# Kernel optimization log

Measured on AMD Instinct MI355X. Metric: run time of the kernel, lower is better.

## Reference

```python
import jax, jax.numpy as jnp
import numpy as np
from math import sqrt

B, S, D_MODEL = 2, 2048, 1024
H = 16
ADIM = D_MODEL // H  # 64
K_REL = 16
N_PEMB = 2 * K_REL + 1  # 33, bidirectional rel-pos vocabulary


def setup_inputs() -> dict:
    key = jax.random.key(0)
    ks = jax.random.split(key, 8)
    sc = 0.02
    return {
        "iQ": jax.random.normal(ks[0], (B, S, D_MODEL), jnp.float32),
        "iK": jax.random.normal(ks[1], (B, S, D_MODEL), jnp.float32),
        "iV": jax.random.normal(ks[2], (B, S, D_MODEL), jnp.float32),
        "Wq": jax.random.normal(ks[3], (D_MODEL, D_MODEL), jnp.float32) * sc,
        "Wk": jax.random.normal(ks[4], (D_MODEL, D_MODEL), jnp.float32) * sc,
        "Wv": jax.random.normal(ks[5], (D_MODEL, D_MODEL), jnp.float32) * sc,
        "Wo": jax.random.normal(ks[6], (D_MODEL, D_MODEL), jnp.float32) * sc,
        "rel_pemb": jax.random.normal(ks[7], (N_PEMB, ADIM), jnp.float32) * sc,
    }


def reference(iQ, iK, iV, Wq, Wk, Wv, Wo, rel_pemb):
    b, nq, _ = iQ.shape
    seql = iK.shape[1]
    # projections -> [b, h, len, d]
    q = (iQ @ Wq).reshape(b, nq, H, ADIM).transpose(0, 2, 1, 3)
    k = (iK @ Wk).reshape(b, seql, H, ADIM).transpose(0, 2, 1, 3)
    v = (iV @ Wv).reshape(b, seql, H, ADIM).transpose(0, 2, 1, 3)
    # content scores: [b, h, nq, seql]
    scores = jnp.einsum("bhqd,bhsd->bhqs", q, k)
    # relative position bias: rel[i, j] = clamp(j - i, -K, K) + K
    pos = jnp.arange(seql)
    rel = jnp.clip(pos[None, :] - pos[:, None], -K_REL, K_REL) + K_REL
    rel = rel[seql - nq:, :]  # narrow to query rows: [nq, seql]
    e = rel_pemb[rel]  # [nq, seql, d]
    scores = scores + jnp.einsum("bhqd,qsd->bhqs", q, e)
    scores = scores / sqrt(ADIM)
    attn = jax.nn.softmax(scores, axis=-1)
    ctx = jnp.einsum("bhqs,bhsd->bqhd", attn, v).reshape(b, nq, H * ADIM)
    return ctx @ Wo
```

## Files before the change

kernel.cpp:

```cpp
#include <hip/hip_runtime.h>
#include <hip/hip_bf16.h>

#define BB 2
#define S 2048
#define DM 1024
#define H 16
#define ADIM 64
#define NP 33

typedef __bf16 bf16x8 __attribute__((ext_vector_type(8)));
typedef float f32x4 __attribute__((ext_vector_type(4)));

__device__ __forceinline__ void gload16(const void* g, void* l) {
  __builtin_amdgcn_global_load_lds(
      (__attribute__((address_space(1))) void*)(g),
      (__attribute__((address_space(3))) void*)(l), 16, 0, 0);
}

__global__ __launch_bounds__(256) void wtrans(
    const float* __restrict__ W0, const float* __restrict__ W1,
    const float* __restrict__ W2, __bf16* __restrict__ T0,
    __bf16* __restrict__ T1, __bf16* __restrict__ T2) {
  const float* W; __bf16* T;
  switch (blockIdx.z) {
    case 0: W = W0; T = T0; break;
    case 1: W = W1; T = T1; break;
    default: W = W2; T = T2; break;
  }
  __shared__ __bf16 tile[64][65];
  int j = threadIdx.x & 63, i0 = threadIdx.x >> 6;
  int n0 = blockIdx.x * 64, k0 = blockIdx.y * 64;
#pragma unroll
  for (int p = 0; p < 16; ++p) {
    int i = i0 + p * 4;
    tile[i][j] = (__bf16)W[(size_t)(k0 + i) * DM + n0 + j];
  }
  __syncthreads();
#pragma unroll
  for (int p = 0; p < 16; ++p) {
    int i = i0 + p * 4;
    T[(size_t)(n0 + i) * DM + k0 + j] = tile[j][i];
  }
}

#define LDK 40
template <bool A_FP32, typename CT>
__device__ __forceinline__ void gemm_body(const void* __restrict__ Av,
                                          const __bf16* __restrict__ BT,
                                          CT* __restrict__ C, int mode) {
  __shared__ __align__(16) __bf16 As[128 * LDK];
  __shared__ __align__(16) __bf16 Bs[128 * 32];
  int t = threadIdx.x;
  int w = t >> 6, lane = t & 63, l15 = lane & 15, quad = lane >> 4;
  int wm = w >> 1, wn = w & 1;
  int i2 = blockIdx.x + (blockIdx.y << 3);
  int xcd = i2 & 7, slot = i2 >> 3;
  int m0 = (xcd + ((slot >> 3) << 3)) * 128;
  int n0 = (slot & 7) * 128;
  constexpr int LA = A_FP32 ? LDK : 32;
  f32x4 acc[4][4] = {};
  int lr = t >> 2;
  int lk = (t & 3) * 8;
  int r4 = lane >> 2;
  int c8 = (lane & 3) * 8;
  for (int k0 = 0; k0 < DM; k0 += 32) {
    if constexpr (A_FP32) {
#pragma unroll
      for (int rr = 0; rr < 2; ++rr) {
        int row = rr * 64 + lr;
        const float* src = (const float*)Av + (size_t)(m0 + row) * DM + k0 + lk;
        float4 a0 = *(const float4*)src;
        float4 a1 = *(const float4*)(src + 4);
        bf16x8 v;
        v[0] = (__bf16)a0.x; v[1] = (__bf16)a0.y;
        v[2] = (__bf16)a0.z; v[3] = (__bf16)a0.w;
        v[4] = (__bf16)a1.x; v[5] = (__bf16)a1.y;
        v[6] = (__bf16)a1.z; v[7] = (__bf16)a1.w;
        *(bf16x8*)&As[row * LDK + lk] = v;
      }
    } else {
#pragma unroll
      for (int q = 0; q < 2; ++q) {
        int half = w * 2 + q;
        gload16((const __bf16*)Av + (size_t)(m0 + half * 16 + r4) * DM + k0 + c8,
                &As[half * 512]);
      }
    }
#pragma unroll
    for (int q = 0; q < 2; ++q) {
      int half = w * 2 + q;
      gload16(&BT[(size_t)(n0 + half * 16 + r4) * DM + k0 + c8],
              &Bs[half * 512]);
    }
    __syncthreads();
    bf16x8 af[4], bfr[4];
#pragma unroll
    for (int mi = 0; mi < 4; ++mi)
      af[mi] = *(const bf16x8*)&As[(wm * 64 + mi * 16 + l15) * LA + quad * 8];
#pragma unroll
    for (int ni = 0; ni < 4; ++ni)
      bfr[ni] = *(const bf16x8*)&Bs[(wn * 64 + ni * 16 + l15) * 32 + quad * 8];
#pragma unroll
    for (int mi = 0; mi < 4; ++mi)
#pragma unroll
      for (int ni = 0; ni < 4; ++ni)
        acc[mi][ni] = __builtin_amdgcn_mfma_f32_16x16x32_bf16(
            af[mi], bfr[ni], acc[mi][ni], 0, 0, 0);
    __syncthreads();
  }
#pragma unroll
  for (int mi = 0; mi < 4; ++mi)
#pragma unroll
    for (int ni = 0; ni < 4; ++ni)
#pragma unroll
      for (int r = 0; r < 4; ++r) {
        int row = m0 + wm * 64 + mi * 16 + quad * 4 + r;
        int col = n0 + wn * 64 + ni * 16 + l15;
        CT v = (CT)acc[mi][ni][r];
        if (mode == 0) {
          C[(size_t)row * DM + col] = v;
        } else {
          int b = row >> 11, s = row & (S - 1);
          int h = col >> 6, d = col & (ADIM - 1);
          if (mode == 1)
            C[((size_t)(b * H + h) * S + s) * ADIM + d] = v;
          else
            C[((size_t)(b * H + h) * ADIM + d) * S + s] = v;
        }
      }
}

__global__ __launch_bounds__(256) void proj3(
    const float* __restrict__ iQ, const float* __restrict__ iK,
    const float* __restrict__ iV, const __bf16* __restrict__ WqT,
    const __bf16* __restrict__ WkT, const __bf16* __restrict__ WvT,
    __bf16* __restrict__ Qw, __bf16* __restrict__ Kw,
    __bf16* __restrict__ Vt) {
  const float* A; const __bf16* B; __bf16* C; int mode;
  switch (blockIdx.z) {
    case 0: A = iQ; B = WqT; C = Qw; mode = 1; break;
    case 1: A = iK; B = WkT; C = Kw; mode = 1; break;
    default: A = iV; B = WvT; C = Vt; mode = 2; break;
  }
  gemm_body<true, __bf16>(A, B, C, mode);
}

__global__ __launch_bounds__(256) void gemm_final(
    const __bf16* __restrict__ ctx, const __bf16* __restrict__ WoT,
    float* __restrict__ out) {
  gemm_body<false, float>(ctx, WoT, out, 0);
}

#define AST 72
__global__ __launch_bounds__(256) void attn_flash(
    const __bf16* __restrict__ Qw, const __bf16* __restrict__ Kw,
    const __bf16* __restrict__ Vt, const float* __restrict__ pemb,
    __bf16* __restrict__ ctx) {
  int bh = blockIdx.y, b = bh >> 4, h = bh & 15;
  int q0 = blockIdx.x * 64;
  int t = threadIdx.x, w = t >> 6, lane = t & 63, l15 = lane & 15,
      quad = lane >> 4;
  const __bf16* Qh = Qw + (size_t)bh * S * ADIM;
  const __bf16* Kh = Kw + (size_t)bh * S * ADIM;
  const __bf16* Vh = Vt + (size_t)bh * ADIM * S;

  __shared__ __align__(16) char smem[36352];
  __bf16* Ks = (__bf16*)smem;
  __bf16* Vs = (__bf16*)(smem + 9216);
  float* pband = (float*)(smem + 18432);
  __bf16* pbufw = (__bf16*)(smem + 27136 + w * 2304);
  __bf16* peb = (__bf16*)smem;

  for (int i = t; i < 48 * 64; i += 256) {
    int r = i >> 6, d = i & 63;
    peb[r * AST + d] = (r < NP) ? (__bf16)pemb[i] : (__bf16)0.f;
  }

  int qa = q0 + w * 16 + l15;
  bf16x8 qf0 = *(const bf16x8*)&Qh[(size_t)qa * ADIM + quad * 8];
  bf16x8 qf1 = *(const bf16x8*)&Qh[(size_t)qa * ADIM + 32 + quad * 8];
  __syncthreads();

  {
    f32x4 pc[3] = {};
#pragma unroll
    for (int ni = 0; ni < 3; ++ni) {
      bf16x8 b0 = *(const bf16x8*)&peb[(ni * 16 + l15) * AST + quad * 8];
      bf16x8 b1 = *(const bf16x8*)&peb[(ni * 16 + l15) * AST + 32 + quad * 8];
      pc[ni] = __builtin_amdgcn_mfma_f32_16x16x32_bf16(qf0, b0, pc[ni], 0, 0, 0);
      pc[ni] = __builtin_amdgcn_mfma_f32_16x16x32_bf16(qf1, b1, pc[ni], 0, 0, 0);
    }
#pragma unroll
    for (int ni = 0; ni < 3; ++ni)
#pragma unroll
      for (int r = 0; r < 4; ++r) {
        int col = ni * 16 + l15;
        if (col < NP) pband[(w * 16 + quad * 4 + r) * 34 + col] = pc[ni][r];
      }
  }
  __syncthreads();

  int qc = q0 + w * 16 + quad * 4;
  int lrow = w * 16 + quad * 4;
  int qw0 = q0 + w * 16;
  float lsum[4] = {0.f, 0.f, 0.f, 0.f};
  f32x4 o[4] = {};

  float blo[4], bhi[4];
#pragma unroll
  for (int r = 0; r < 4; ++r) {
    blo[r] = __expf(pband[(lrow + r) * 34 + 0] * 0.125f);
    bhi[r] = __expf(pband[(lrow + r) * 34 + 32] * 0.125f);
  }

  int srow = t >> 3;
  int scol = (t & 7) * 8;
  bf16x8 k0r = *(const bf16x8*)&Kh[(size_t)srow * ADIM + scol];
  bf16x8 k1r = *(const bf16x8*)&Kh[(size_t)(32 + srow) * ADIM + scol];
  bf16x8 v0r = *(const bf16x8*)&Vh[(size_t)srow * S + scol];
  bf16x8 v1r = *(const bf16x8*)&Vh[(size_t)(32 + srow) * S + scol];

  for (int s0 = 0; s0 < S; s0 += 64) {
    __syncthreads();
    *(bf16x8*)&Ks[srow * AST + scol] = k0r;
    *(bf16x8*)&Ks[(32 + srow) * AST + scol] = k1r;
    *(bf16x8*)&Vs[srow * AST + scol] = v0r;
    *(bf16x8*)&Vs[(32 + srow) * AST + scol] = v1r;
    int sn = s0 + 64;
    if (sn < S) {
      k0r = *(const bf16x8*)&Kh[(size_t)(sn + srow) * ADIM + scol];
      k1r = *(const bf16x8*)&Kh[(size_t)(sn + 32 + srow) * ADIM + scol];
      v0r = *(const bf16x8*)&Vh[(size_t)srow * S + sn + scol];
      v1r = *(const bf16x8*)&Vh[(size_t)(32 + srow) * S + sn + scol];
    }
    __syncthreads();

    f32x4 c[4];
#pragma unroll
    for (int j = 0; j < 4; ++j) {
      f32x4 cj = {};
      bf16x8 kb0 = *(const bf16x8*)&Ks[(j * 16 + l15) * AST + quad * 8];
      bf16x8 kb1 = *(const bf16x8*)&Ks[(j * 16 + l15) * AST + 32 + quad * 8];
      cj = __builtin_amdgcn_mfma_f32_16x16x32_bf16(qf0, kb0, cj, 0, 0, 0);
      cj = __builtin_amdgcn_mfma_f32_16x16x32_bf16(qf1, kb1, cj, 0, 0, 0);
      c[j] = cj;
    }

    float pv[4][4];
    bool below = (s0 + 79 <= qw0);
    bool above = (s0 >= qw0 + 31);
    if (below || above) {
#pragma unroll
      for (int j = 0; j < 4; ++j)
#pragma unroll
        for (int r = 0; r < 4; ++r) {
          float f = below ? blo[r] : bhi[r];
          float e = __expf(c[j][r] * 0.125f) * f;
          lsum[r] += e;
          pv[j][r] = e;
        }
    } else {
#pragma unroll
      for (int j = 0; j < 4; ++j)
#pragma unroll
        for (int r = 0; r < 4; ++r) {
          int qg = qc + r;
          int sg = s0 + j * 16 + l15;
          int i0 = sg - qg; i0 = i0 < -16 ? -16 : (i0 > 16 ? 16 : i0); i0 += 16;
          float e = __expf((c[j][r] + pband[(lrow + r) * 34 + i0]) * 0.125f);
          lsum[r] += e;
          pv[j][r] = e;
        }
    }

#pragma unroll
    for (int j = 0; j < 4; ++j)
#pragma unroll
      for (int r = 0; r < 4; ++r)
        pbufw[(quad * 4 + r) * AST + j * 16 + l15] = (__bf16)pv[j][r];
    bf16x8 pa0 = *(const bf16x8*)&pbufw[l15 * AST + quad * 8];
    bf16x8 pa1 = *(const bf16x8*)&pbufw[l15 * AST + 32 + quad * 8];

#pragma unroll
    for (int nt = 0; nt < 4; ++nt) {
      bf16x8 vb0 = *(const bf16x8*)&Vs[(nt * 16 + l15) * AST + quad * 8];
      bf16x8 vb1 = *(const bf16x8*)&Vs[(nt * 16 + l15) * AST + 32 + quad * 8];
      o[nt] = __builtin_amdgcn_mfma_f32_16x16x32_bf16(pa0, vb0, o[nt], 0, 0, 0);
      o[nt] = __builtin_amdgcn_mfma_f32_16x16x32_bf16(pa1, vb1, o[nt], 0, 0, 0);
    }
  }

#pragma unroll
  for (int r = 0; r < 4; ++r) {
#pragma unroll
    for (int mm = 1; mm < 16; mm <<= 1) lsum[r] += __shfl_xor(lsum[r], mm, 64);
  }
#pragma unroll
  for (int nt = 0; nt < 4; ++nt)
#pragma unroll
    for (int r = 0; r < 4; ++r) {
      int qg = qc + r;
      int d = nt * 16 + l15;
      ctx[(size_t)(b * S + qg) * DM + h * ADIM + d] =
          (__bf16)(o[nt][r] / lsum[r]);
    }
}

extern "C" void kernel_launch(void* const* d_in, const int* in_sizes, int n_in,
                              void* d_out, int out_size, void* d_ws,
                              size_t ws_size, hipStream_t stream) {
  bool sizes_ok =
      (n_in == 8 && in_sizes[0] == BB * S * DM && in_sizes[1] == BB * S * DM &&
       in_sizes[2] == BB * S * DM && in_sizes[3] == DM * DM &&
       in_sizes[4] == DM * DM && in_sizes[5] == DM * DM &&
       in_sizes[6] == DM * DM && in_sizes[7] == NP * ADIM &&
       out_size == BB * S * DM);
  if (!sizes_ok) return;
  if (ws_size < 33ull * 1024 * 1024) return;

  const float* iQ = (const float*)d_in[0];
  const float* iK = (const float*)d_in[1];
  const float* iV = (const float*)d_in[2];
  const float* Wq = (const float*)d_in[3];
  const float* Wk = (const float*)d_in[4];
  const float* Wv = (const float*)d_in[5];
  const float* Wo = (const float*)d_in[6];
  const float* pemb = (const float*)d_in[7];

  char* w = (char*)d_ws;
  const size_t MB = 1024 * 1024;
  __bf16* Qw  = (__bf16*)(w + 0 * MB);
  __bf16* Kw  = (__bf16*)(w + 8 * MB);
  __bf16* Vt  = (__bf16*)(w + 16 * MB);
  __bf16* ctx = (__bf16*)(w + 24 * MB);
  __bf16* WqT = (__bf16*)(w + 24 * MB);
  __bf16* WkT = (__bf16*)(w + 26 * MB);
  __bf16* WvT = (__bf16*)(w + 28 * MB);
  __bf16* WoT = (__bf16*)(w + 0 * MB);

  wtrans<<<dim3(16, 16, 3), 256, 0, stream>>>(Wq, Wk, Wv, WqT, WkT, WvT);
  proj3<<<dim3(8, 32, 3), 256, 0, stream>>>(iQ, iK, iV, WqT, WkT, WvT,
                                            Qw, Kw, Vt);
  attn_flash<<<dim3(S / 64, BB * H), 256, 0, stream>>>(Qw, Kw, Vt, pemb, ctx);
  wtrans<<<dim3(16, 16, 1), 256, 0, stream>>>(Wo, Wo, Wo, WoT, WoT, WoT);
  gemm_final<<<dim3(8, 32), 256, 0, stream>>>(ctx, WoT, (float*)d_out);
}
```

Before: 266.9 us.

## Load K/V MFMA fragments directly from global, drop LDS staging and barriers

Removes the shared-memory staging of K and V tiles along with the two per-iteration __syncthreads, so each wave now loads its MFMA operand fragments straight from global memory (relying on L1/L2 for reuse across the four waves). It also folds the 1/sqrt(d) scale and the band bias into an exp2 with a premultiplied log2e constant and an FMA. Dropping the LDS buffers shrinks shared memory, which may raise occupancy. The cost is that each wave now fetches K/V from global four times with no software prefetch, so load latency is exposed.

```diff
diff --git a/kernel.cpp b/kernel.cpp
--- a/kernel.cpp
+++ b/kernel.cpp
@@ -164,12 +164,10 @@
   const __bf16* Kh = Kw + (size_t)bh * S * ADIM;
   const __bf16* Vh = Vt + (size_t)bh * ADIM * S;
 
-  __shared__ __align__(16) char smem[36352];
-  __bf16* Ks = (__bf16*)smem;
-  __bf16* Vs = (__bf16*)(smem + 9216);
-  float* pband = (float*)(smem + 18432);
-  __bf16* pbufw = (__bf16*)(smem + 27136 + w * 2304);
+  __shared__ __align__(16) char smem[24832];
   __bf16* peb = (__bf16*)smem;
+  float* pband = (float*)(smem + 6912);
+  __bf16* pbufw = (__bf16*)(smem + 15616 + w * 2304);
 
   for (int i = t; i < 48 * 64; i += 256) {
     int r = i >> 6, d = i & 63;
@@ -206,43 +204,36 @@
   float lsum[4] = {0.f, 0.f, 0.f, 0.f};
   f32x4 o[4] = {};
 
-  float blo[4], bhi[4];
+  const float K2 = 0.18033688011112f;
+  float pK0[4], pK32[4];
 #pragma unroll
   for (int r = 0; r < 4; ++r) {
-    blo[r] = __expf(pband[(lrow + r) * 34 + 0] * 0.125f);
-    bhi[r] = __expf(pband[(lrow + r) * 34 + 32] * 0.125f);
-  }
-
-  int srow = t >> 3;
-  int scol = (t & 7) * 8;
-  bf16x8 k0r = *(const bf16x8*)&Kh[(size_t)srow * ADIM + scol];
-  bf16x8 k1r = *(const bf16x8*)&Kh[(size_t)(32 + srow) * ADIM + scol];
-  bf16x8 v0r = *(const bf16x8*)&Vh[(size_t)srow * S + scol];
-  bf16x8 v1r = *(const bf16x8*)&Vh[(size_t)(32 + srow) * S + scol];
+    pK0[r] = pband[(lrow + r) * 34 + 0] * K2;
+    pK32[r] = pband[(lrow + r) * 34 + 32] * K2;
+  }
 
   for (int s0 = 0; s0 < S; s0 += 64) {
-    __syncthreads();
-    *(bf16x8*)&Ks[srow * AST + scol] = k0r;
-    *(bf16x8*)&Ks[(32 + srow) * AST + scol] = k1r;
-    *(bf16x8*)&Vs[srow * AST + scol] = v0r;
-    *(bf16x8*)&Vs[(32 + srow) * AST + scol] = v1r;
-    int sn = s0 + 64;
-    if (sn < S) {
-      k0r = *(const bf16x8*)&Kh[(size_t)(sn + srow) * ADIM + scol];
-      k1r = *(const bf16x8*)&Kh[(size_t)(sn + 32 + srow) * ADIM + scol];
-      v0r = *(const bf16x8*)&Vh[(size_t)srow * S + sn + scol];
-      v1r = *(const bf16x8*)&Vh[(size_t)(32 + srow) * S + sn + scol];
-    }
-    __syncthreads();
+    const __bf16* Kt = Kh + (size_t)s0 * ADIM;
+    bf16x8 kb0[4], kb1[4];
+#pragma unroll
+    for (int j = 0; j < 4; ++j) {
+      kb0[j] = *(const bf16x8*)&Kt[(size_t)(j * 16 + l15) * ADIM + quad * 8];
+      kb1[j] = *(const bf16x8*)&Kt[(size_t)(j * 16 + l15) * ADIM + 32 + quad * 8];
+    }
+    bf16x8 vb0[4], vb1[4];
+#pragma unroll
+    for (int nt = 0; nt < 4; ++nt) {
+      vb0[nt] = *(const bf16x8*)&Vh[(size_t)(nt * 16 + l15) * S + s0 + quad * 8];
+      vb1[nt] =
+          *(const bf16x8*)&Vh[(size_t)(nt * 16 + l15) * S + s0 + 32 + quad * 8];
+    }
 
     f32x4 c[4];
 #pragma unroll
     for (int j = 0; j < 4; ++j) {
       f32x4 cj = {};
-      bf16x8 kb0 = *(const bf16x8*)&Ks[(j * 16 + l15) * AST + quad * 8];
-      bf16x8 kb1 = *(const bf16x8*)&Ks[(j * 16 + l15) * AST + 32 + quad * 8];
-      cj = __builtin_amdgcn_mfma_f32_16x16x32_bf16(qf0, kb0, cj, 0, 0, 0);
-      cj = __builtin_amdgcn_mfma_f32_16x16x32_bf16(qf1, kb1, cj, 0, 0, 0);
+      cj = __builtin_amdgcn_mfma_f32_16x16x32_bf16(qf0, kb0[j], cj, 0, 0, 0);
+      cj = __builtin_amdgcn_mfma_f32_16x16x32_bf16(qf1, kb1[j], cj, 0, 0, 0);
       c[j] = cj;
     }
 
@@ -254,8 +245,8 @@
       for (int j = 0; j < 4; ++j)
 #pragma unroll
         for (int r = 0; r < 4; ++r) {
-          float f = below ? blo[r] : bhi[r];
-          float e = __expf(c[j][r] * 0.125f) * f;
+          float pk = below ? pK0[r] : pK32[r];
+          float e = exp2f(__builtin_fmaf(c[j][r], K2, pk));
           lsum[r] += e;
           pv[j][r] = e;
         }
@@ -267,7 +258,7 @@
           int qg = qc + r;
           int sg = s0 + j * 16 + l15;
           int i0 = sg - qg; i0 = i0 < -16 ? -16 : (i0 > 16 ? 16 : i0); i0 += 16;
-          float e = __expf((c[j][r] + pband[(lrow + r) * 34 + i0]) * 0.125f);
+          float e = exp2f((c[j][r] + pband[(lrow + r) * 34 + i0]) * K2);
           lsum[r] += e;
           pv[j][r] = e;
         }
@@ -283,10 +274,8 @@
 
 #pragma unroll
     for (int nt = 0; nt < 4; ++nt) {
-      bf16x8 vb0 = *(const bf16x8*)&Vs[(nt * 16 + l15) * AST + quad * 8];
-      bf16x8 vb1 = *(const bf16x8*)&Vs[(nt * 16 + l15) * AST + 32 + quad * 8];
-      o[nt] = __builtin_amdgcn_mfma_f32_16x16x32_bf16(pa0, vb0, o[nt], 0, 0, 0);
-      o[nt] = __builtin_amdgcn_mfma_f32_16x16x32_bf16(pa1, vb1, o[nt], 0, 0, 0);
+      o[nt] = __builtin_amdgcn_mfma_f32_16x16x32_bf16(pa0, vb0[nt], o[nt], 0, 0, 0);
+      o[nt] = __builtin_amdgcn_mfma_f32_16x16x32_bf16(pa1, vb1[nt], o[nt], 0, 0, 0);
     }
   }
 
```

Measured after the change: 422.7 us. +58.4%, slower.

## Double query rows per attention block and narrow output GEMM tile to 64 columns

Applied to the files above, without the earlier changes.

The attention kernel now gives each wave 32 query rows (two 16-row groups) instead of 16, so each K/V tile loaded into shared memory feeds twice the MFMA work and half as many blocks are launched. The softmax exponent switches to exp2 with a folded log2e/sqrt(d) constant and an FMA for the off-band case. The output projection GEMM is templated to a 128x64 tile with a new XCD-aware block mapping, doubling its grid for better CU occupancy. The trade-offs are more registers and shared memory per attention block, which lowers occupancy, and fewer attention blocks, which may underfill the GPU.

```diff
diff --git a/kernel.cpp b/kernel.cpp
--- a/kernel.cpp
+++ b/kernel.cpp
@@ -44,21 +44,20 @@
 }
 
 #define LDK 40
-template <bool A_FP32, typename CT>
+template <bool A_FP32, int BN, typename CT>
 __device__ __forceinline__ void gemm_body(const void* __restrict__ Av,
                                           const __bf16* __restrict__ BT,
-                                          CT* __restrict__ C, int mode) {
+                                          CT* __restrict__ C, int mode,
+                                          int m0, int n0) {
+  constexpr int NF = BN / 32;
+  constexpr int BH = BN / 16;
   __shared__ __align__(16) __bf16 As[128 * LDK];
-  __shared__ __align__(16) __bf16 Bs[128 * 32];
+  __shared__ __align__(16) __bf16 Bs[BN * 32];
   int t = threadIdx.x;
   int w = t >> 6, lane = t & 63, l15 = lane & 15, quad = lane >> 4;
   int wm = w >> 1, wn = w & 1;
-  int i2 = blockIdx.x + (blockIdx.y << 3);
-  int xcd = i2 & 7, slot = i2 >> 3;
-  int m0 = (xcd + ((slot >> 3) << 3)) * 128;
-  int n0 = (slot & 7) * 128;
   constexpr int LA = A_FP32 ? LDK : 32;
-  f32x4 acc[4][4] = {};
+  f32x4 acc[4][NF] = {};
   int lr = t >> 2;
   int lk = (t & 3) * 8;
   int r4 = lane >> 2;
@@ -87,23 +86,24 @@
       }
     }
 #pragma unroll
-    for (int q = 0; q < 2; ++q) {
-      int half = w * 2 + q;
+    for (int q = 0; q < BH / 4; ++q) {
+      int half = w * (BH / 4) + q;
       gload16(&BT[(size_t)(n0 + half * 16 + r4) * DM + k0 + c8],
               &Bs[half * 512]);
     }
     __syncthreads();
-    bf16x8 af[4], bfr[4];
+    bf16x8 af[4], bfr[NF];
 #pragma unroll
     for (int mi = 0; mi < 4; ++mi)
       af[mi] = *(const bf16x8*)&As[(wm * 64 + mi * 16 + l15) * LA + quad * 8];
 #pragma unroll
-    for (int ni = 0; ni < 4; ++ni)
-      bfr[ni] = *(const bf16x8*)&Bs[(wn * 64 + ni * 16 + l15) * 32 + quad * 8];
+    for (int ni = 0; ni < NF; ++ni)
+      bfr[ni] =
+          *(const bf16x8*)&Bs[(wn * (BN / 2) + ni * 16 + l15) * 32 + quad * 8];
 #pragma unroll
     for (int mi = 0; mi < 4; ++mi)
 #pragma unroll
-      for (int ni = 0; ni < 4; ++ni)
+      for (int ni = 0; ni < NF; ++ni)
         acc[mi][ni] = __builtin_amdgcn_mfma_f32_16x16x32_bf16(
             af[mi], bfr[ni], acc[mi][ni], 0, 0, 0);
     __syncthreads();
@@ -111,11 +111,11 @@
 #pragma unroll
   for (int mi = 0; mi < 4; ++mi)
 #pragma unroll
-    for (int ni = 0; ni < 4; ++ni)
+    for (int ni = 0; ni < NF; ++ni)
 #pragma unroll
       for (int r = 0; r < 4; ++r) {
         int row = m0 + wm * 64 + mi * 16 + quad * 4 + r;
-        int col = n0 + wn * 64 + ni * 16 + l15;
+        int col = n0 + wn * (BN / 2) + ni * 16 + l15;
         CT v = (CT)acc[mi][ni][r];
         if (mode == 0) {
           C[(size_t)row * DM + col] = v;
@@ -142,13 +142,21 @@
     case 1: A = iK; B = WkT; C = Kw; mode = 1; break;
     default: A = iV; B = WvT; C = Vt; mode = 2; break;
   }
-  gemm_body<true, __bf16>(A, B, C, mode);
+  int i2 = blockIdx.x + (blockIdx.y << 3);
+  int xcd = i2 & 7, slot = i2 >> 3;
+  int m0 = (xcd + ((slot >> 3) << 3)) * 128;
+  int n0 = (slot & 7) * 128;
+  gemm_body<true, 128, __bf16>(A, B, C, mode, m0, n0);
 }
 
 __global__ __launch_bounds__(256) void gemm_final(
     const __bf16* __restrict__ ctx, const __bf16* __restrict__ WoT,
     float* __restrict__ out) {
-  gemm_body<false, float>(ctx, WoT, out, 0);
+  int i2 = blockIdx.x + (blockIdx.y << 4);
+  int xcd = i2 & 7, slot = i2 >> 3;
+  int m0 = ((xcd << 2) + (slot >> 4)) * 128;
+  int n0 = (slot & 15) * 64;
+  gemm_body<false, 64, float>(ctx, WoT, out, 0, m0, n0);
 }
 
 #define AST 72
@@ -157,18 +165,17 @@
     const __bf16* __restrict__ Vt, const float* __restrict__ pemb,
     __bf16* __restrict__ ctx) {
   int bh = blockIdx.y, b = bh >> 4, h = bh & 15;
-  int q0 = blockIdx.x * 64;
+  int q0 = blockIdx.x * 128;
   int t = threadIdx.x, w = t >> 6, lane = t & 63, l15 = lane & 15,
       quad = lane >> 4;
   const __bf16* Qh = Qw + (size_t)bh * S * ADIM;
   const __bf16* Kh = Kw + (size_t)bh * S * ADIM;
   const __bf16* Vh = Vt + (size_t)bh * ADIM * S;
 
-  __shared__ __align__(16) char smem[36352];
+  __shared__ __align__(16) char smem[54272];
   __bf16* Ks = (__bf16*)smem;
   __bf16* Vs = (__bf16*)(smem + 9216);
   float* pband = (float*)(smem + 18432);
-  __bf16* pbufw = (__bf16*)(smem + 27136 + w * 2304);
   __bf16* peb = (__bf16*)smem;
 
   for (int i = t; i < 48 * 64; i += 256) {
@@ -176,42 +183,52 @@
     peb[r * AST + d] = (r < NP) ? (__bf16)pemb[i] : (__bf16)0.f;
   }
 
-  int qa = q0 + w * 16 + l15;
-  bf16x8 qf0 = *(const bf16x8*)&Qh[(size_t)qa * ADIM + quad * 8];
-  bf16x8 qf1 = *(const bf16x8*)&Qh[(size_t)qa * ADIM + 32 + quad * 8];
+  bf16x8 qf[2][2];
+#pragma unroll
+  for (int g = 0; g < 2; ++g) {
+    int qa = q0 + w * 32 + g * 16 + l15;
+    qf[g][0] = *(const bf16x8*)&Qh[(size_t)qa * ADIM + quad * 8];
+    qf[g][1] = *(const bf16x8*)&Qh[(size_t)qa * ADIM + 32 + quad * 8];
+  }
   __syncthreads();
 
-  {
+#pragma unroll
+  for (int g = 0; g < 2; ++g) {
     f32x4 pc[3] = {};
 #pragma unroll
     for (int ni = 0; ni < 3; ++ni) {
       bf16x8 b0 = *(const bf16x8*)&peb[(ni * 16 + l15) * AST + quad * 8];
       bf16x8 b1 = *(const bf16x8*)&peb[(ni * 16 + l15) * AST + 32 + quad * 8];
-      pc[ni] = __builtin_amdgcn_mfma_f32_16x16x32_bf16(qf0, b0, pc[ni], 0, 0, 0);
-      pc[ni] = __builtin_amdgcn_mfma_f32_16x16x32_bf16(qf1, b1, pc[ni], 0, 0, 0);
+      pc[ni] =
+          __builtin_amdgcn_mfma_f32_16x16x32_bf16(qf[g][0], b0, pc[ni], 0, 0, 0);
+      pc[ni] =
+          __builtin_amdgcn_mfma_f32_16x16x32_bf16(qf[g][1], b1, pc[ni], 0, 0, 0);
     }
 #pragma unroll
     for (int ni = 0; ni < 3; ++ni)
 #pragma unroll
       for (int r = 0; r < 4; ++r) {
         int col = ni * 16 + l15;
-        if (col < NP) pband[(w * 16 + quad * 4 + r) * 34 + col] = pc[ni][r];
+        if (col < NP)
+          pband[(w * 32 + g * 16 + quad * 4 + r) * 34 + col] = pc[ni][r];
       }
   }
   __syncthreads();
 
-  int qc = q0 + w * 16 + quad * 4;
-  int lrow = w * 16 + quad * 4;
-  int qw0 = q0 + w * 16;
-  float lsum[4] = {0.f, 0.f, 0.f, 0.f};
-  f32x4 o[4] = {};
-
-  float blo[4], bhi[4];
-#pragma unroll
-  for (int r = 0; r < 4; ++r) {
-    blo[r] = __expf(pband[(lrow + r) * 34 + 0] * 0.125f);
-    bhi[r] = __expf(pband[(lrow + r) * 34 + 32] * 0.125f);
-  }
+  int qw0 = q0 + w * 32;
+  float lsum[2][4] = {};
+  f32x4 o[2][4] = {};
+
+  const float K2 = 0.18033688011112f;
+  float pK0[2][4], pK32[2][4];
+#pragma unroll
+  for (int g = 0; g < 2; ++g)
+#pragma unroll
+    for (int r = 0; r < 4; ++r) {
+      int lrow = w * 32 + g * 16 + quad * 4 + r;
+      pK0[g][r] = pband[lrow * 34 + 0] * K2;
+      pK32[g][r] = pband[lrow * 34 + 32] * K2;
+    }
 
   int srow = t >> 3;
   int scol = (t & 7) * 8;
@@ -235,75 +252,100 @@
     }
     __syncthreads();
 
-    f32x4 c[4];
+    f32x4 c[2][4];
 #pragma unroll
     for (int j = 0; j < 4; ++j) {
-      f32x4 cj = {};
       bf16x8 kb0 = *(const bf16x8*)&Ks[(j * 16 + l15) * AST + quad * 8];
       bf16x8 kb1 = *(const bf16x8*)&Ks[(j * 16 + l15) * AST + 32 + quad * 8];
-      cj = __builtin_amdgcn_mfma_f32_16x16x32_bf16(qf0, kb0, cj, 0, 0, 0);
-      cj = __builtin_amdgcn_mfma_f32_16x16x32_bf16(qf1, kb1, cj, 0, 0, 0);
-      c[j] = cj;
-    }
-
-    float pv[4][4];
-    bool below = (s0 + 79 <= qw0);
-    bool above = (s0 >= qw0 + 31);
-    if (below || above) {
+#pragma unroll
+      for (int g = 0; g < 2; ++g) {
+        f32x4 cj = {};
+        cj = __builtin_amdgcn_mfma_f32_16x16x32_bf16(qf[g][0], kb0, cj, 0, 0, 0);
+        cj = __builtin_amdgcn_mfma_f32_16x16x32_bf16(qf[g][1], kb1, cj, 0, 0, 0);
+        c[g][j] = cj;
+      }
+    }
+
+    float pv[2][4][4];
+#pragma unroll
+    for (int g = 0; g < 2; ++g) {
+      int qg0 = qw0 + g * 16;
+      bool below = (s0 + 79 <= qg0);
+      bool above = (s0 >= qg0 + 31);
+      if (below || above) {
+#pragma unroll
+        for (int j = 0; j < 4; ++j)
+#pragma unroll
+          for (int r = 0; r < 4; ++r) {
+            float pk = below ? pK0[g][r] : pK32[g][r];
+            float e = exp2f(__builtin_fmaf(c[g][j][r], K2, pk));
+            lsum[g][r] += e;
+            pv[g][j][r] = e;
+          }
+      } else {
+#pragma unroll
+        for (int j = 0; j < 4; ++j)
+#pragma unroll
+          for (int r = 0; r < 4; ++r) {
+            int qg = qg0 + quad * 4 + r;
+            int sg = s0 + j * 16 + l15;
+            int i0 = sg - qg;
+            i0 = i0 < -16 ? -16 : (i0 > 16 ? 16 : i0);
+            i0 += 16;
+            int lrow = w * 32 + g * 16 + quad * 4 + r;
+            float e = exp2f((c[g][j][r] + pband[lrow * 34 + i0]) * K2);
+            lsum[g][r] += e;
+            pv[g][j][r] = e;
+          }
+      }
+    }
+
+    bf16x8 pa0[2], pa1[2];
+#pragma unroll
+    for (int g = 0; g < 2; ++g) {
+      __bf16* pb = (__bf16*)(smem + 35840 + (w * 2 + g) * 2304);
 #pragma unroll
       for (int j = 0; j < 4; ++j)
 #pragma unroll
-        for (int r = 0; r < 4; ++r) {
-          float f = below ? blo[r] : bhi[r];
-          float e = __expf(c[j][r] * 0.125f) * f;
-          lsum[r] += e;
-          pv[j][r] = e;
-        }
-    } else {
-#pragma unroll
-      for (int j = 0; j < 4; ++j)
-#pragma unroll
-        for (int r = 0; r < 4; ++r) {
-          int qg = qc + r;
-          int sg = s0 + j * 16 + l15;
-          int i0 = sg - qg; i0 = i0 < -16 ? -16 : (i0 > 16 ? 16 : i0); i0 += 16;
-          float e = __expf((c[j][r] + pband[(lrow + r) * 34 + i0]) * 0.125f);
-          lsum[r] += e;
-          pv[j][r] = e;
-        }
-    }
-
-#pragma unroll
-    for (int j = 0; j < 4; ++j)
-#pragma unroll
-      for (int r = 0; r < 4; ++r)
-        pbufw[(quad * 4 + r) * AST + j * 16 + l15] = (__bf16)pv[j][r];
-    bf16x8 pa0 = *(const bf16x8*)&pbufw[l15 * AST + quad * 8];
-    bf16x8 pa1 = *(const bf16x8*)&pbufw[l15 * AST + 32 + quad * 8];
+        for (int r = 0; r < 4; ++r)
+          pb[(quad * 4 + r) * AST + j * 16 + l15] = (__bf16)pv[g][j][r];
+      pa0[g] = *(const bf16x8*)&pb[l15 * AST + quad * 8];
+      pa1[g] = *(const bf16x8*)&pb[l15 * AST + 32 + quad * 8];
+    }
 
 #pragma unroll
     for (int nt = 0; nt < 4; ++nt) {
       bf16x8 vb0 = *(const bf16x8*)&Vs[(nt * 16 + l15) * AST + quad * 8];
       bf16x8 vb1 = *(const bf16x8*)&Vs[(nt * 16 + l15) * AST + 32 + quad * 8];
-      o[nt] = __builtin_amdgcn_mfma_f32_16x16x32_bf16(pa0, vb0, o[nt], 0, 0, 0);
-      o[nt] = __builtin_amdgcn_mfma_f32_16x16x32_bf16(pa1, vb1, o[nt], 0, 0, 0);
-    }
-  }
-
-#pragma unroll
-  for (int r = 0; r < 4; ++r) {
-#pragma unroll
-    for (int mm = 1; mm < 16; mm <<= 1) lsum[r] += __shfl_xor(lsum[r], mm, 64);
-  }
-#pragma unroll
-  for (int nt = 0; nt < 4; ++nt)
+#pragma unroll
+      for (int g = 0; g < 2; ++g) {
+        o[g][nt] =
+            __builtin_amdgcn_mfma_f32_16x16x32_bf16(pa0[g], vb0, o[g][nt], 0, 0, 0);
+        o[g][nt] =
+            __builtin_amdgcn_mfma_f32_16x16x32_bf16(pa1[g], vb1, o[g][nt], 0, 0, 0);
+      }
+    }
+  }
+
+#pragma unroll
+  for (int g = 0; g < 2; ++g)
 #pragma unroll
     for (int r = 0; r < 4; ++r) {
-      int qg = qc + r;
-      int d = nt * 16 + l15;
-      ctx[(size_t)(b * S + qg) * DM + h * ADIM + d] =
-          (__bf16)(o[nt][r] / lsum[r]);
-    }
+#pragma unroll
+      for (int mm = 1; mm < 16; mm <<= 1)
+        lsum[g][r] += __shfl_xor(lsum[g][r], mm, 64);
+    }
+#pragma unroll
+  for (int g = 0; g < 2; ++g)
+#pragma unroll
+    for (int nt = 0; nt < 4; ++nt)
+#pragma unroll
+      for (int r = 0; r < 4; ++r) {
+        int qg = q0 + w * 32 + g * 16 + quad * 4 + r;
+        int d = nt * 16 + l15;
+        ctx[(size_t)(b * S + qg) * DM + h * ADIM + d] =
+            (__bf16)(o[g][nt][r] / lsum[g][r]);
+      }
 }
 
 extern "C" void kernel_launch(void* const* d_in, const int* in_sizes, int n_in,
@@ -341,7 +383,7 @@
   wtrans<<<dim3(16, 16, 3), 256, 0, stream>>>(Wq, Wk, Wv, WqT, WkT, WvT);
   proj3<<<dim3(8, 32, 3), 256, 0, stream>>>(iQ, iK, iV, WqT, WkT, WvT,
                                             Qw, Kw, Vt);
-  attn_flash<<<dim3(S / 64, BB * H), 256, 0, stream>>>(Qw, Kw, Vt, pemb, ctx);
+  attn_flash<<<dim3(S / 128, BB * H), 256, 0, stream>>>(Qw, Kw, Vt, pemb, ctx);
   wtrans<<<dim3(16, 16, 1), 256, 0, stream>>>(Wo, Wo, Wo, WoT, WoT, WoT);
-  gemm_final<<<dim3(8, 32), 256, 0, stream>>>(ctx, WoT, (float*)d_out);
-}
+  gemm_final<<<dim3(16, 32), 256, 0, stream>>>(ctx, WoT, (float*)d_out);
+}
```

Result: no change. 269.7 us (+1.0%).
